# Kernel tuning notes

Hardware: AMD Instinct MI355X
Metric: run time of the kernel (lower is better)

Reference implementation:

```python
import jax, jax.numpy as jnp
import numpy as np

N = 4096
IN_DIM = 256
OUT_DIM = 256
NUM_HEADS = 4
HEAD_DIM = OUT_DIM // NUM_HEADS


def setup_inputs() -> dict:
    key = jax.random.key(0)
    ks = jax.random.split(key, 10)
    x = jax.random.normal(ks[0], (N, IN_DIM), dtype=jnp.float32)
    adj = jax.random.randint(ks[1], (N, N), 0, 2, dtype=jnp.int32)
    adj = jnp.maximum(adj, jnp.eye(N, dtype=jnp.int32))  # self-loops -> no empty rows
    s_in = 1.0 / np.sqrt(IN_DIM)
    s_out = 1.0 / np.sqrt(OUT_DIM)
    Wq = jax.random.uniform(ks[2], (IN_DIM, OUT_DIM), jnp.float32, -s_in, s_in)
    bq = jnp.zeros((OUT_DIM,), jnp.float32)
    Wk = jax.random.uniform(ks[3], (IN_DIM, OUT_DIM), jnp.float32, -s_in, s_in)
    bk = jnp.zeros((OUT_DIM,), jnp.float32)
    Wv = jax.random.uniform(ks[4], (IN_DIM, OUT_DIM), jnp.float32, -s_in, s_in)
    bv = jnp.zeros((OUT_DIM,), jnp.float32)
    Wo = jax.random.uniform(ks[5], (OUT_DIM, OUT_DIM), jnp.float32, -s_out, s_out)
    bo = jnp.zeros((OUT_DIM,), jnp.float32)
    gamma = jnp.ones((OUT_DIM,), jnp.float32)
    beta = jnp.zeros((OUT_DIM,), jnp.float32)
    return {"x": x, "adj": adj, "Wq": Wq, "bq": bq, "Wk": Wk, "bk": bk,
            "Wv": Wv, "bv": bv, "Wo": Wo, "bo": bo, "gamma": gamma, "beta": beta}


def layer_norm(h, gamma, beta, eps=1e-5):
    mu = jnp.mean(h, axis=-1, keepdims=True)
    var = jnp.mean(jnp.square(h - mu), axis=-1, keepdims=True)
    return (h - mu) * jax.lax.rsqrt(var + eps) * gamma + beta


def reference(x, adj, Wq, bq, Wk, bk, Wv, bv, Wo, bo, gamma, beta):
    n = x.shape[0]
    q_proj = x @ Wq + bq                       # (N, out_dim), reused for residual
    Q = q_proj.reshape(n, NUM_HEADS, HEAD_DIM)
    K = (x @ Wk + bk).reshape(n, NUM_HEADS, HEAD_DIM)
    V = (x @ Wv + bv).reshape(n, NUM_HEADS, HEAD_DIM)
    scores = jnp.einsum('nhd,mhd->nmh', Q, K) / np.sqrt(HEAD_DIM)
    scores = jnp.where(adj[:, :, None] == 0, -jnp.inf, scores)
    attn = jax.nn.softmax(scores, axis=1)      # softmax over neighbor axis m
    out = jnp.einsum('nmh,mhd->nhd', attn, V).reshape(n, OUT_DIM)
    out = out @ Wo + bo
    return layer_norm(out + q_proj, gamma, beta)
```

## Files before the change

kernel.cpp:

```cpp
#include <hip/hip_runtime.h>
#include <math.h>

#define NN 4096
#define DIM 256
#define NHEADS 4
#define HDIM 64

typedef short bf16x8 __attribute__((ext_vector_type(8)));
typedef float f32x4  __attribute__((ext_vector_type(4)));

__device__ __forceinline__ unsigned short f2bf(float f) {
    unsigned int u = __float_as_uint(f);
    u += 0x7fffu + ((u >> 16) & 1u);
    return (unsigned short)(u >> 16);
}
__device__ __forceinline__ float bf2f(unsigned short h) {
    return __uint_as_float(((unsigned int)h) << 16);
}
__device__ __forceinline__ void async16(const void* g, void* l) {
    __builtin_amdgcn_global_load_lds(
        (const __attribute__((address_space(1))) unsigned int*)g,
        (__attribute__((address_space(3))) unsigned int*)l, 16, 0, 0);
}

__global__ __launch_bounds__(256)
void prep_kernel(const float* __restrict__ W0, const float* __restrict__ W1,
                 const float* __restrict__ W2, const float* __restrict__ W3,
                 unsigned short* __restrict__ T0, unsigned short* __restrict__ T1,
                 unsigned short* __restrict__ T2, unsigned short* __restrict__ T3)
{
    __shared__ unsigned short Ts[64][65];
    const int b = blockIdx.x, t = threadIdx.x;
    const int mat = b >> 4, tile = b & 15;
    const int r0 = (tile >> 2) * 64, c0 = (tile & 3) * 64;
    const float* W = (mat == 0) ? W0 : (mat == 1) ? W1 : (mat == 2) ? W2 : W3;
    unsigned short* T = (mat == 0) ? T0 : (mat == 1) ? T1 : (mat == 2) ? T2 : T3;
    {
        int r = t >> 2, c4 = (t & 3) * 16;
        #pragma unroll
        for (int j = 0; j < 4; ++j) {
            float4 v = *reinterpret_cast<const float4*>(W + (size_t)(r0 + r) * DIM + c0 + c4 + j * 4);
            Ts[c4 + j * 4 + 0][r] = f2bf(v.x);
            Ts[c4 + j * 4 + 1][r] = f2bf(v.y);
            Ts[c4 + j * 4 + 2][r] = f2bf(v.z);
            Ts[c4 + j * 4 + 3][r] = f2bf(v.w);
        }
    }
    __syncthreads();
    {
        int d = t >> 2, k4 = (t & 3) * 16;
        #pragma unroll
        for (int j = 0; j < 4; ++j) {
            ushort4 u;
            u.x = Ts[d][k4 + j * 4 + 0];
            u.y = Ts[d][k4 + j * 4 + 1];
            u.z = Ts[d][k4 + j * 4 + 2];
            u.w = Ts[d][k4 + j * 4 + 3];
            *reinterpret_cast<ushort4*>(T + (size_t)(c0 + d) * DIM + r0 + k4 + j * 4) = u;
        }
    }
}

__global__ __launch_bounds__(256)
void qkv_mask(const float* __restrict__ x,
              const unsigned short* __restrict__ WqT, const unsigned short* __restrict__ WkT,
              const unsigned short* __restrict__ WvT,
              const float* __restrict__ bq, const float* __restrict__ bk, const float* __restrict__ bv,
              unsigned short* __restrict__ Qo, unsigned short* __restrict__ Ko,
              unsigned short* __restrict__ VTo,
              const int* __restrict__ adj, unsigned long long* __restrict__ maskT)
{
    const int b = blockIdx.x, t = threadIdx.x, w = t >> 6, l = t & 63;

    if (b >= 384) {
        const int ww = (b - 384) * 4 + w;
        for (int idx = ww; idx < 65536; idx += 8192) {
            const int row = idx >> 4, st = idx & 15;
            const int4 a = *reinterpret_cast<const int4*>(adj + (size_t)row * NN + st * 256 + l * 4);
            unsigned long long b0 = __ballot(a.x != 0);
            unsigned long long b1 = __ballot(a.y != 0);
            unsigned long long b2 = __ballot(a.z != 0);
            unsigned long long b3 = __ballot(a.w != 0);
            if (l < 4) {
                unsigned long long bb = (l == 0) ? b0 : (l == 1) ? b1 : (l == 2) ? b2 : b3;
                maskT[((size_t)st * 4 + l) * NN + row] = bb;
            }
        }
        return;
    }

    const int l15 = l & 15, lg = l >> 4;
    const int which = b >> 7, xb = b & 127;
    const int row0 = xb * 32 + (w >> 1) * 16;
    const int col0 = (w & 1) * 128;
    const unsigned short* WT; const float* bias;
    if (which == 0)      { WT = WqT; bias = bq; }
    else if (which == 1) { WT = WkT; bias = bk; }
    else                 { WT = WvT; bias = bv; }

    f32x4 acc[8] = {};
    for (int k0 = 0; k0 < DIM; k0 += 32) {
        const float* xp = x + (size_t)(row0 + l15) * DIM + k0 + lg * 8;
        float4 x0 = *reinterpret_cast<const float4*>(xp);
        float4 x1 = *reinterpret_cast<const float4*>(xp + 4);
        union { unsigned u[4]; bf16x8 v; } xa;
        asm("v_cvt_pk_bf16_f32 %0, %1, %2" : "=v"(xa.u[0]) : "v"(x0.x), "v"(x0.y));
        asm("v_cvt_pk_bf16_f32 %0, %1, %2" : "=v"(xa.u[1]) : "v"(x0.z), "v"(x0.w));
        asm("v_cvt_pk_bf16_f32 %0, %1, %2" : "=v"(xa.u[2]) : "v"(x1.x), "v"(x1.y));
        asm("v_cvt_pk_bf16_f32 %0, %1, %2" : "=v"(xa.u[3]) : "v"(x1.z), "v"(x1.w));
        #pragma unroll
        for (int nt = 0; nt < 8; ++nt) {
            bf16x8 wb = *(const bf16x8*)(WT + (size_t)(col0 + nt * 16 + l15) * DIM + k0 + lg * 8);
            acc[nt] = __builtin_amdgcn_mfma_f32_16x16x32_bf16(xa.v, wb, acc[nt], 0, 0, 0);
        }
    }
    #pragma unroll
    for (int nt = 0; nt < 8; ++nt) {
        int col = col0 + nt * 16 + l15;
        float bb = bias[col];
        #pragma unroll
        for (int r = 0; r < 4; ++r) {
            int row = row0 + lg * 4 + r;
            unsigned short val = f2bf(acc[nt][r] + bb);
            if (which == 2) {
                int prow = (row & ~63) | (((row & 15) << 2) | ((row >> 4) & 3));
                VTo[(size_t)col * NN + prow] = val;
            } else if (which == 0) Qo[(size_t)row * DIM + col] = val;
            else                   Ko[(size_t)row * DIM + col] = val;
        }
    }
}

template<int NTILES>
__global__ __launch_bounds__(256)
void attn_mfma(const unsigned short* __restrict__ Qb, const unsigned short* __restrict__ Kb,
               const unsigned short* __restrict__ VT, const unsigned long long* __restrict__ maskT,
               unsigned short* __restrict__ Opart, float* __restrict__ lpart)
{
    constexpr int NSTR = NTILES / 4;
    __shared__ unsigned short Kt[2][64][64];
    __shared__ unsigned short Vt[2][64][64];
    __shared__ unsigned short Pb[4][32][64];

    const int t = threadIdx.x, w = t >> 6, l = t & 63, l15 = l & 15, lg = l >> 4;
    const int n0 = blockIdx.x * 128, h = blockIdx.y, sp = blockIdx.z;
    const int kv_base = sp * NTILES * 64;
    const int qbase = n0 + w * 32;

    bf16x8 qa[2][2];
    #pragma unroll
    for (int sub = 0; sub < 2; ++sub) {
        const unsigned short* qp = Qb + (size_t)(qbase + sub * 16 + l15) * DIM + h * HDIM + lg * 8;
        qa[sub][0] = *(const bf16x8*)(qp);
        qa[sub][1] = *(const bf16x8*)(qp + 32);
    }

    const int srow  = w * 16 + (l >> 3);
    const int sunit = (l & 7) ^ (srow & 7);
    const unsigned short* kS = Kb + (size_t)(kv_base + srow) * DIM + h * HDIM + sunit * 8;
    const unsigned short* vS = VT + (size_t)(h * HDIM + srow) * NN + kv_base + sunit * 8;

    const int xr  = l15 & 7;
    const int ko0 = (lg ^ xr) << 4;
    const int ko1 = ((4 + lg) ^ xr) << 4;
    const int s0  = l15 >> 2;

    const short onev = (l15 == 0) ? (short)0x3F80 : (short)0;
    const bf16x8 onesb = {onev, onev, onev, onev, onev, onev, onev, onev};

    f32x4 oa[2][4] = {};
    f32x4 os[2] = {};

    {
        unsigned short* kd = &Kt[0][w * 16][0];
        unsigned short* vd = &Vt[0][w * 16][0];
        async16(kS,           kd);
        async16(kS + 8 * DIM, kd + 8 * 64);
        async16(vS,           vd);
        async16(vS + 8 * NN,  vd + 8 * 64);
    }

    char* const pbase = (char*)&Pb[w][0][0];

    #pragma unroll
    for (int st = 0; st < NSTR; ++st) {
        unsigned lo[2][4], hi[2][4];
        #pragma unroll
        for (int sub = 0; sub < 2; ++sub) {
            ulonglong4 m4 = *reinterpret_cast<const ulonglong4*>(
                maskT + ((size_t)((kv_base >> 8) + st) * 4 + (l15 & 3)) * NN + qbase + sub * 16 + lg * 4);
            lo[sub][0] = (unsigned)m4.x; hi[sub][0] = (unsigned)(m4.x >> 32);
            lo[sub][1] = (unsigned)m4.y; hi[sub][1] = (unsigned)(m4.y >> 32);
            lo[sub][2] = (unsigned)m4.z; hi[sub][2] = (unsigned)(m4.z >> 32);
            lo[sub][3] = (unsigned)m4.w; hi[sub][3] = (unsigned)(m4.w >> 32);
        }

        #pragma unroll
        for (int m = 0; m < 4; ++m) {
            const int tl = st * 4 + m;
            const int bsel = tl & 1;
            if (tl + 1 < NTILES) {
                const unsigned short* ks = kS + (size_t)(tl + 1) * 64 * DIM;
                const unsigned short* vs = vS + (tl + 1) * 64;
                unsigned short* kd = &Kt[bsel ^ 1][w * 16][0];
                unsigned short* vd = &Vt[bsel ^ 1][w * 16][0];
                async16(ks,           kd);
                async16(ks + 8 * DIM, kd + 8 * 64);
                async16(vs,           vd);
                async16(vs + 8 * NN,  vd + 8 * 64);
                asm volatile("s_waitcnt vmcnt(4)" ::: "memory");
            } else {
                asm volatile("s_waitcnt vmcnt(0)" ::: "memory");
            }
            __builtin_amdgcn_s_barrier();
            __builtin_amdgcn_sched_barrier(0);

            const char* kbase = (const char*)&Kt[bsel][0][0] + l15 * 128;
            const char* vbase = (const char*)&Vt[bsel][0][0] + l15 * 128;

            f32x4 sa[2][4] = {};
            __builtin_amdgcn_s_setprio(1);
            #pragma unroll
            for (int nt = 0; nt < 4; ++nt) {
                bf16x8 kb0 = *(const bf16x8*)(kbase + nt * 2048 + ko0);
                bf16x8 kb1 = *(const bf16x8*)(kbase + nt * 2048 + ko1);
                #pragma unroll
                for (int sub = 0; sub < 2; ++sub) {
                    sa[sub][nt] = __builtin_amdgcn_mfma_f32_16x16x32_bf16(qa[sub][0], kb0, sa[sub][nt], 0, 0, 0);
                    sa[sub][nt] = __builtin_amdgcn_mfma_f32_16x16x32_bf16(qa[sub][1], kb1, sa[sub][nt], 0, 0, 0);
                }
            }
            __builtin_amdgcn_s_setprio(0);

            #pragma unroll
            for (int sub = 0; sub < 2; ++sub) {
                #pragma unroll
                for (int r = 0; r < 4; ++r) {
                    const unsigned sel = (m & 2) ? hi[sub][r] : lo[sub][r];
                    const int sh0 = ((m & 1) << 4) + s0;
                    float p0, p1, p2, p3;
                    {
                        unsigned bit = (sel >> (sh0 + 0)) & 1u;
                        p0 = exp2f(bit ? sa[sub][0][r] * 0.18033688f : -INFINITY);
                    }
                    {
                        unsigned bit = (sel >> (sh0 + 4)) & 1u;
                        p1 = exp2f(bit ? sa[sub][1][r] * 0.18033688f : -INFINITY);
                    }
                    {
                        unsigned bit = (sel >> (sh0 + 8)) & 1u;
                        p2 = exp2f(bit ? sa[sub][2][r] * 0.18033688f : -INFINITY);
                    }
                    {
                        unsigned bit = (sel >> (sh0 + 12)) & 1u;
                        p3 = exp2f(bit ? sa[sub][3][r] * 0.18033688f : -INFINITY);
                    }
                    unsigned u01, u23;
                    asm("v_cvt_pk_bf16_f32 %0, %1, %2" : "=v"(u01) : "v"(p0), "v"(p1));
                    asm("v_cvt_pk_bf16_f32 %0, %1, %2" : "=v"(u23) : "v"(p2), "v"(p3));
                    const int rr = sub * 16 + lg * 4 + r;
                    *reinterpret_cast<uint2*>(pbase + rr * 128 +
                        ((((l15 >> 1) ^ (rr & 7)) << 4) | ((l15 & 1) << 3))) = make_uint2(u01, u23);
                }
            }

            bf16x8 pa[2][2];
            #pragma unroll
            for (int sub = 0; sub < 2; ++sub) {
                pa[sub][0] = *(const bf16x8*)(pbase + (sub * 16 + l15) * 128 + ko0);
                pa[sub][1] = *(const bf16x8*)(pbase + (sub * 16 + l15) * 128 + ko1);
            }

            __builtin_amdgcn_s_setprio(1);
            #pragma unroll
            for (int nt = 0; nt < 4; ++nt) {
                bf16x8 vb0 = *(const bf16x8*)(vbase + nt * 2048 + ko0);
                bf16x8 vb1 = *(const bf16x8*)(vbase + nt * 2048 + ko1);
                #pragma unroll
                for (int sub = 0; sub < 2; ++sub) {
                    oa[sub][nt] = __builtin_amdgcn_mfma_f32_16x16x32_bf16(pa[sub][0], vb0, oa[sub][nt], 0, 0, 0);
                    oa[sub][nt] = __builtin_amdgcn_mfma_f32_16x16x32_bf16(pa[sub][1], vb1, oa[sub][nt], 0, 0, 0);
                }
            }
            #pragma unroll
            for (int sub = 0; sub < 2; ++sub) {
                os[sub] = __builtin_amdgcn_mfma_f32_16x16x32_bf16(pa[sub][0], onesb, os[sub], 0, 0, 0);
                os[sub] = __builtin_amdgcn_mfma_f32_16x16x32_bf16(pa[sub][1], onesb, os[sub], 0, 0, 0);
            }
            __builtin_amdgcn_s_setprio(0);

            __builtin_amdgcn_sched_barrier(0);
            __builtin_amdgcn_s_barrier();
        }
    }

    #pragma unroll
    for (int sub = 0; sub < 2; ++sub) {
        #pragma unroll
        for (int r = 0; r < 4; ++r) {
            const int qr = qbase + sub * 16 + lg * 4 + r;
            #pragma unroll
            for (int nt = 0; nt < 4; ++nt)
                Opart[((size_t)sp * NN + qr) * DIM + h * HDIM + nt * 16 + l15] = f2bf(oa[sub][nt][r]);
            if (l15 == 0)
                lpart[((size_t)sp * NN + qr) * NHEADS + h] = os[sub][r];
        }
    }
}

__global__ __launch_bounds__(256)
void combine_kernel(const unsigned short* __restrict__ Opart, const float* __restrict__ lpart,
                    unsigned short* __restrict__ AOb, int S)
{
    const int tid = blockIdx.x * blockDim.x + threadIdx.x;
    const int q  = tid >> 6;
    const int d  = (tid & 63) * 4;
    const int h  = d >> 6;
    float o0 = 0.f, o1 = 0.f, o2 = 0.f, o3 = 0.f, lsum = 0.f;
    for (int s = 0; s < S; ++s) {
        ushort4 u = *reinterpret_cast<const ushort4*>(Opart + ((size_t)s * NN + q) * DIM + d);
        o0 += bf2f(u.x); o1 += bf2f(u.y); o2 += bf2f(u.z); o3 += bf2f(u.w);
        lsum += lpart[((size_t)s * NN + q) * NHEADS + h];
    }
    float inv = 1.f / lsum;
    ushort4 o;
    o.x = f2bf(o0 * inv); o.y = f2bf(o1 * inv); o.z = f2bf(o2 * inv); o.w = f2bf(o3 * inv);
    *reinterpret_cast<ushort4*>(AOb + (size_t)q * DIM + d) = o;
}

__global__ __launch_bounds__(256)
void out_ln(const unsigned short* __restrict__ Ab, const unsigned short* __restrict__ WoT,
            const float* __restrict__ bo, const unsigned short* __restrict__ Rb,
            const float* __restrict__ gamma, const float* __restrict__ beta,
            float* __restrict__ out)
{
    __shared__ float redsum[4][16];
    __shared__ float redsq[4][16];
    const int t = threadIdx.x, w = t >> 6, l = t & 63, l15 = l & 15, lg = l >> 4;
    const int row0 = blockIdx.x * 16;
    const int col0 = w * 64;

    f32x4 acc[4] = {};
    for (int k0 = 0; k0 < DIM; k0 += 32) {
        bf16x8 xa = *(const bf16x8*)(Ab + (size_t)(row0 + l15) * DIM + k0 + lg * 8);
        #pragma unroll
        for (int nt = 0; nt < 4; ++nt) {
            bf16x8 wb = *(const bf16x8*)(WoT + (size_t)(col0 + nt * 16 + l15) * DIM + k0 + lg * 8);
            acc[nt] = __builtin_amdgcn_mfma_f32_16x16x32_bf16(xa, wb, acc[nt], 0, 0, 0);
        }
    }

    float psum[4] = {0, 0, 0, 0}, psq[4] = {0, 0, 0, 0};
    #pragma unroll
    for (int nt = 0; nt < 4; ++nt) {
        int col = col0 + nt * 16 + l15;
        float bb = bo[col];
        #pragma unroll
        for (int r = 0; r < 4; ++r) {
            int row = row0 + lg * 4 + r;
            float xv = acc[nt][r] + bb + bf2f(Rb[(size_t)row * DIM + col]);
            acc[nt][r] = xv;
            psum[r] += xv; psq[r] += xv * xv;
        }
    }
    #pragma unroll
    for (int r = 0; r < 4; ++r) {
        float s = psum[r], q = psq[r];
        s += __shfl_xor(s, 1); q += __shfl_xor(q, 1);
        s += __shfl_xor(s, 2); q += __shfl_xor(q, 2);
        s += __shfl_xor(s, 4); q += __shfl_xor(q, 4);
        s += __shfl_xor(s, 8); q += __shfl_xor(q, 8);
        psum[r] = s; psq[r] = q;
    }
    if (l15 == 0) {
        #pragma unroll
        for (int r = 0; r < 4; ++r) {
            redsum[w][lg * 4 + r] = psum[r];
            redsq[w][lg * 4 + r]  = psq[r];
        }
    }
    __syncthreads();

    float msave[4], rsave[4];
    #pragma unroll
    for (int r = 0; r < 4; ++r) {
        int row = lg * 4 + r;
        float s = redsum[0][row] + redsum[1][row] + redsum[2][row] + redsum[3][row];
        float q = redsq[0][row] + redsq[1][row] + redsq[2][row] + redsq[3][row];
        float mean = s * (1.f / 256.f);
        float var  = q * (1.f / 256.f) - mean * mean;
        msave[r] = mean;
        rsave[r] = rsqrtf(var + 1e-5f);
    }
    #pragma unroll
    for (int nt = 0; nt < 4; ++nt) {
        int col = col0 + nt * 16 + l15;
        float g = gamma[col], bt = beta[col];
        #pragma unroll
        for (int r = 0; r < 4; ++r) {
            int row = row0 + lg * 4 + r;
            out[(size_t)row * DIM + col] = (acc[nt][r] - msave[r]) * rsave[r] * g + bt;
        }
    }
}

extern "C" void kernel_launch(void* const* d_in, const int* in_sizes, int n_in,
                              void* d_out, int out_size, void* d_ws, size_t ws_size,
                              hipStream_t stream) {
    const float* x     = (const float*)d_in[0];
    const int*   adj   = (const int*)  d_in[1];
    const float* Wq    = (const float*)d_in[2];
    const float* bq    = (const float*)d_in[3];
    const float* Wk    = (const float*)d_in[4];
    const float* bk    = (const float*)d_in[5];
    const float* Wv    = (const float*)d_in[6];
    const float* bv    = (const float*)d_in[7];
    const float* Wo    = (const float*)d_in[8];
    const float* bo    = (const float*)d_in[9];
    const float* gamma = (const float*)d_in[10];
    const float* beta  = (const float*)d_in[11];
    float* out = (float*)d_out;

    char* ws = (char*)d_ws;
    const size_t MB = 1u << 20;
    unsigned short*     Qb    = (unsigned short*)(ws + 0 * MB);
    unsigned short*     Kb    = (unsigned short*)(ws + 2 * MB);
    unsigned short*     VT    = (unsigned short*)(ws + 4 * MB);
    unsigned long long* maskT = (unsigned long long*)(ws + 6 * MB);
    unsigned short*     WqT   = (unsigned short*)(ws + 8 * MB);
    unsigned short*     WkT   = (unsigned short*)(ws + 8 * MB + 128 * 1024);
    unsigned short*     WvT   = (unsigned short*)(ws + 8 * MB + 256 * 1024);
    unsigned short*     WoT   = (unsigned short*)(ws + 8 * MB + 384 * 1024);
    unsigned short*     AOb   = (unsigned short*)(ws + 8 * MB + 512 * 1024);
    float*              lpart = (float*)(ws + 10 * MB + 512 * 1024);
    unsigned short*     Opart = (unsigned short*)(ws + 11 * MB);

    const int S = (ws_size >= 27 * MB) ? 8 : 4;

    prep_kernel<<<64, 256, 0, stream>>>(Wq, Wk, Wv, Wo, WqT, WkT, WvT, WoT);

    qkv_mask<<<384 + 2048, 256, 0, stream>>>(
        x, WqT, WkT, WvT, bq, bk, bv, Qb, Kb, VT, adj, maskT);

    if (S == 8)
        attn_mfma<8><<<dim3(NN / 128, NHEADS, 8), 256, 0, stream>>>(
            Qb, Kb, VT, maskT, Opart, lpart);
    else
        attn_mfma<16><<<dim3(NN / 128, NHEADS, 4), 256, 0, stream>>>(
            Qb, Kb, VT, maskT, Opart, lpart);

    combine_kernel<<<NN * DIM / 4 / 256, 256, 0, stream>>>(Opart, lpart, AOb, S);

    out_ln<<<NN / 16, 256, 0, stream>>>(AOb, WoT, bo, Qb, gamma, beta, out);
}
```

Measured before the change: 89.58 us.

## Compute transposed scores so P feeds PV MFMA from registers without LDS

Swaps the MFMA operand order in the QK^T product so each lane holds score columns in the layout the PV MFMA needs as its A operand. The probabilities are packed straight into registers, which removes the per-wave LDS round trip through Pb. The mask is stored row-major per query and V is re-permuted so the layouts match. The row sums move from extra MFMAs against a ones vector to scalar adds plus a shuffle reduction. The risk is subtle permutation mismatches and extra VALU register pressure.

```diff
diff --git a/kernel.cpp b/kernel.cpp
--- a/kernel.cpp
+++ b/kernel.cpp
@@ -83,7 +83,7 @@
             unsigned long long b3 = __ballot(a.w != 0);
             if (l < 4) {
                 unsigned long long bb = (l == 0) ? b0 : (l == 1) ? b1 : (l == 2) ? b2 : b3;
-                maskT[((size_t)st * 4 + l) * NN + row] = bb;
+                maskT[(size_t)row * 64 + st * 4 + l] = bb;
             }
         }
         return;
@@ -123,8 +123,10 @@
             int row = row0 + lg * 4 + r;
             unsigned short val = f2bf(acc[nt][r] + bb);
             if (which == 2) {
-                int prow = (row & ~63) | (((row & 15) << 2) | ((row >> 4) & 3));
-                VTo[(size_t)col * NN + prow] = val;
+                int rb = row & 63;
+                int vnt = rb >> 4, vlg = (rb >> 2) & 3, vr = rb & 3;
+                int pos = ((vnt & 1) << 5) | (vlg << 3) | ((vnt >> 1) << 2) | vr;
+                VTo[(size_t)col * NN + ((row & ~63) | pos)] = val;
             } else if (which == 0) Qo[(size_t)row * DIM + col] = val;
             else                   Ko[(size_t)row * DIM + col] = val;
         }
@@ -140,7 +142,6 @@
     constexpr int NSTR = NTILES / 4;
     __shared__ unsigned short Kt[2][64][64];
     __shared__ unsigned short Vt[2][64][64];
-    __shared__ unsigned short Pb[4][32][64];
 
     const int t = threadIdx.x, w = t >> 6, l = t & 63, l15 = l & 15, lg = l >> 4;
     const int n0 = blockIdx.x * 128, h = blockIdx.y, sp = blockIdx.z;
@@ -155,6 +156,9 @@
         qa[sub][1] = *(const bf16x8*)(qp + 32);
     }
 
+    const unsigned long long* mbase0 = maskT + (size_t)(qbase + l15) * 64 + (kv_base >> 6);
+    const unsigned long long* mbase1 = maskT + (size_t)(qbase + 16 + l15) * 64 + (kv_base >> 6);
+
     const int srow  = w * 16 + (l >> 3);
     const int sunit = (l & 7) ^ (srow & 7);
     const unsigned short* kS = Kb + (size_t)(kv_base + srow) * DIM + h * HDIM + sunit * 8;
@@ -163,13 +167,9 @@
     const int xr  = l15 & 7;
     const int ko0 = (lg ^ xr) << 4;
     const int ko1 = ((4 + lg) ^ xr) << 4;
-    const int s0  = l15 >> 2;
-
-    const short onev = (l15 == 0) ? (short)0x3F80 : (short)0;
-    const bf16x8 onesb = {onev, onev, onev, onev, onev, onev, onev, onev};
 
     f32x4 oa[2][4] = {};
-    f32x4 os[2] = {};
+    float lsum[2] = {0.f, 0.f};
 
     {
         unsigned short* kd = &Kt[0][w * 16][0];
@@ -180,20 +180,19 @@
         async16(vS + 8 * NN,  vd + 8 * 64);
     }
 
-    char* const pbase = (char*)&Pb[w][0][0];
-
     #pragma unroll
     for (int st = 0; st < NSTR; ++st) {
+        ulonglong4 m40 = *reinterpret_cast<const ulonglong4*>(mbase0 + st * 4);
+        ulonglong4 m41 = *reinterpret_cast<const ulonglong4*>(mbase1 + st * 4);
         unsigned lo[2][4], hi[2][4];
-        #pragma unroll
-        for (int sub = 0; sub < 2; ++sub) {
-            ulonglong4 m4 = *reinterpret_cast<const ulonglong4*>(
-                maskT + ((size_t)((kv_base >> 8) + st) * 4 + (l15 & 3)) * NN + qbase + sub * 16 + lg * 4);
-            lo[sub][0] = (unsigned)m4.x; hi[sub][0] = (unsigned)(m4.x >> 32);
-            lo[sub][1] = (unsigned)m4.y; hi[sub][1] = (unsigned)(m4.y >> 32);
-            lo[sub][2] = (unsigned)m4.z; hi[sub][2] = (unsigned)(m4.z >> 32);
-            lo[sub][3] = (unsigned)m4.w; hi[sub][3] = (unsigned)(m4.w >> 32);
-        }
+        lo[0][0] = (unsigned)m40.x; hi[0][0] = (unsigned)(m40.x >> 32);
+        lo[0][1] = (unsigned)m40.y; hi[0][1] = (unsigned)(m40.y >> 32);
+        lo[0][2] = (unsigned)m40.z; hi[0][2] = (unsigned)(m40.z >> 32);
+        lo[0][3] = (unsigned)m40.w; hi[0][3] = (unsigned)(m40.w >> 32);
+        lo[1][0] = (unsigned)m41.x; hi[1][0] = (unsigned)(m41.x >> 32);
+        lo[1][1] = (unsigned)m41.y; hi[1][1] = (unsigned)(m41.y >> 32);
+        lo[1][2] = (unsigned)m41.z; hi[1][2] = (unsigned)(m41.z >> 32);
+        lo[1][3] = (unsigned)m41.w; hi[1][3] = (unsigned)(m41.w >> 32);
 
         #pragma unroll
         for (int m = 0; m < 4; ++m) {
@@ -226,49 +225,43 @@
                 bf16x8 kb1 = *(const bf16x8*)(kbase + nt * 2048 + ko1);
                 #pragma unroll
                 for (int sub = 0; sub < 2; ++sub) {
-                    sa[sub][nt] = __builtin_amdgcn_mfma_f32_16x16x32_bf16(qa[sub][0], kb0, sa[sub][nt], 0, 0, 0);
-                    sa[sub][nt] = __builtin_amdgcn_mfma_f32_16x16x32_bf16(qa[sub][1], kb1, sa[sub][nt], 0, 0, 0);
+                    sa[sub][nt] = __builtin_amdgcn_mfma_f32_16x16x32_bf16(kb0, qa[sub][0], sa[sub][nt], 0, 0, 0);
+                    sa[sub][nt] = __builtin_amdgcn_mfma_f32_16x16x32_bf16(kb1, qa[sub][1], sa[sub][nt], 0, 0, 0);
                 }
             }
             __builtin_amdgcn_s_setprio(0);
 
-            #pragma unroll
-            for (int sub = 0; sub < 2; ++sub) {
-                #pragma unroll
-                for (int r = 0; r < 4; ++r) {
-                    const unsigned sel = (m & 2) ? hi[sub][r] : lo[sub][r];
-                    const int sh0 = ((m & 1) << 4) + s0;
-                    float p0, p1, p2, p3;
-                    {
-                        unsigned bit = (sel >> (sh0 + 0)) & 1u;
-                        p0 = exp2f(bit ? sa[sub][0][r] * 0.18033688f : -INFINITY);
-                    }
-                    {
-                        unsigned bit = (sel >> (sh0 + 4)) & 1u;
-                        p1 = exp2f(bit ? sa[sub][1][r] * 0.18033688f : -INFINITY);
-                    }
-                    {
-                        unsigned bit = (sel >> (sh0 + 8)) & 1u;
-                        p2 = exp2f(bit ? sa[sub][2][r] * 0.18033688f : -INFINITY);
-                    }
-                    {
-                        unsigned bit = (sel >> (sh0 + 12)) & 1u;
-                        p3 = exp2f(bit ? sa[sub][3][r] * 0.18033688f : -INFINITY);
-                    }
-                    unsigned u01, u23;
-                    asm("v_cvt_pk_bf16_f32 %0, %1, %2" : "=v"(u01) : "v"(p0), "v"(p1));
-                    asm("v_cvt_pk_bf16_f32 %0, %1, %2" : "=v"(u23) : "v"(p2), "v"(p3));
-                    const int rr = sub * 16 + lg * 4 + r;
-                    *reinterpret_cast<uint2*>(pbase + rr * 128 +
-                        ((((l15 >> 1) ^ (rr & 7)) << 4) | ((l15 & 1) << 3))) = make_uint2(u01, u23);
-                }
-            }
-
+            const int bsh = ((m & 1) << 4) + lg;
             bf16x8 pa[2][2];
             #pragma unroll
             for (int sub = 0; sub < 2; ++sub) {
-                pa[sub][0] = *(const bf16x8*)(pbase + (sub * 16 + l15) * 128 + ko0);
-                pa[sub][1] = *(const bf16x8*)(pbase + (sub * 16 + l15) * 128 + ko1);
+                unsigned s0 = ((m & 2) ? hi[sub][0] : lo[sub][0]) >> bsh;
+                unsigned s1 = ((m & 2) ? hi[sub][1] : lo[sub][1]) >> bsh;
+                unsigned s2 = ((m & 2) ? hi[sub][2] : lo[sub][2]) >> bsh;
+                unsigned s3 = ((m & 2) ? hi[sub][3] : lo[sub][3]) >> bsh;
+                float p[4][4];
+                #pragma unroll
+                for (int nt = 0; nt < 4; ++nt) {
+                    p[nt][0] = exp2f(((s0 >> (nt * 4)) & 1u) ? sa[sub][nt][0] * 0.18033688f : -INFINITY);
+                    p[nt][1] = exp2f(((s1 >> (nt * 4)) & 1u) ? sa[sub][nt][1] * 0.18033688f : -INFINITY);
+                    p[nt][2] = exp2f(((s2 >> (nt * 4)) & 1u) ? sa[sub][nt][2] * 0.18033688f : -INFINITY);
+                    p[nt][3] = exp2f(((s3 >> (nt * 4)) & 1u) ? sa[sub][nt][3] * 0.18033688f : -INFINITY);
+                }
+                lsum[sub] += (((p[0][0] + p[0][1]) + (p[0][2] + p[0][3])) +
+                              ((p[1][0] + p[1][1]) + (p[1][2] + p[1][3]))) +
+                             (((p[2][0] + p[2][1]) + (p[2][2] + p[2][3])) +
+                              ((p[3][0] + p[3][1]) + (p[3][2] + p[3][3])));
+                union { unsigned u[4]; bf16x8 v; } a0, a1;
+                asm("v_cvt_pk_bf16_f32 %0, %1, %2" : "=v"(a0.u[0]) : "v"(p[0][0]), "v"(p[0][1]));
+                asm("v_cvt_pk_bf16_f32 %0, %1, %2" : "=v"(a0.u[1]) : "v"(p[0][2]), "v"(p[0][3]));
+                asm("v_cvt_pk_bf16_f32 %0, %1, %2" : "=v"(a0.u[2]) : "v"(p[2][0]), "v"(p[2][1]));
+                asm("v_cvt_pk_bf16_f32 %0, %1, %2" : "=v"(a0.u[3]) : "v"(p[2][2]), "v"(p[2][3]));
+                asm("v_cvt_pk_bf16_f32 %0, %1, %2" : "=v"(a1.u[0]) : "v"(p[1][0]), "v"(p[1][1]));
+                asm("v_cvt_pk_bf16_f32 %0, %1, %2" : "=v"(a1.u[1]) : "v"(p[1][2]), "v"(p[1][3]));
+                asm("v_cvt_pk_bf16_f32 %0, %1, %2" : "=v"(a1.u[2]) : "v"(p[3][0]), "v"(p[3][1]));
+                asm("v_cvt_pk_bf16_f32 %0, %1, %2" : "=v"(a1.u[3]) : "v"(p[3][2]), "v"(p[3][3]));
+                pa[sub][0] = a0.v;
+                pa[sub][1] = a1.v;
             }
 
             __builtin_amdgcn_s_setprio(1);
@@ -282,11 +275,6 @@
                     oa[sub][nt] = __builtin_amdgcn_mfma_f32_16x16x32_bf16(pa[sub][1], vb1, oa[sub][nt], 0, 0, 0);
                 }
             }
-            #pragma unroll
-            for (int sub = 0; sub < 2; ++sub) {
-                os[sub] = __builtin_amdgcn_mfma_f32_16x16x32_bf16(pa[sub][0], onesb, os[sub], 0, 0, 0);
-                os[sub] = __builtin_amdgcn_mfma_f32_16x16x32_bf16(pa[sub][1], onesb, os[sub], 0, 0, 0);
-            }
             __builtin_amdgcn_s_setprio(0);
 
             __builtin_amdgcn_sched_barrier(0);
@@ -296,14 +284,17 @@
 
     #pragma unroll
     for (int sub = 0; sub < 2; ++sub) {
+        float v = lsum[sub];
+        v += __shfl_xor(v, 16);
+        v += __shfl_xor(v, 32);
+        if (lg == 0)
+            lpart[((size_t)sp * NN + qbase + sub * 16 + l15) * NHEADS + h] = v;
         #pragma unroll
         for (int r = 0; r < 4; ++r) {
             const int qr = qbase + sub * 16 + lg * 4 + r;
             #pragma unroll
             for (int nt = 0; nt < 4; ++nt)
                 Opart[((size_t)sp * NN + qr) * DIM + h * HDIM + nt * 16 + l15] = f2bf(oa[sub][nt][r]);
-            if (l15 == 0)
-                lpart[((size_t)sp * NN + qr) * NHEADS + h] = os[sub][r];
         }
     }
 }
```

Result: no change. 90.74 us (+1.3%).
